# Optimization experiments

Measured on AMD Instinct MI355X. Metric: run time of the kernel, lower is better.

Reference implementation:

```python
import jax, jax.numpy as jnp
from jax import lax
import numpy as np

DEPTH = 10  # matches init depth; n_nodes = 2**DEPTH - 1 = 1023


def setup_inputs() -> dict:
    key = jax.random.key(0)
    k1, k2, k3 = jax.random.split(key, 3)
    B, nIn, nOut = 65536, 1024, 1024
    n_nodes = 2 ** DEPTH - 1
    x = jax.random.normal(k1, (B, nIn), dtype=jnp.float32)
    # hyperspherical-shell init: unit-normalized gaussian rows
    w1s = jax.random.normal(k2, (n_nodes, nIn), dtype=jnp.float32)
    w1s = w1s / jnp.linalg.norm(w1s, axis=-1, keepdims=True)
    w2s = jax.random.normal(k3, (n_nodes, nOut), dtype=jnp.float32)
    w2s = w2s / jnp.linalg.norm(w2s, axis=-1, keepdims=True)
    return {"x": x, "w1s": w1s, "w2s": w2s}


def reference(x, w1s, w2s):
    B = x.shape[0]
    nOut = w2s.shape[1]

    def step(carry, _):
        node, y = carry                      # node: [B] int32, y: [B, nOut]
        lam = jnp.einsum('bi,bi->b', x, w1s[node])      # per-sample dot
        y = y + lam[:, None] * w2s[node]                 # accumulate scaled leaf vec
        node = node * 2 + 1 + (lam > 0).astype(node.dtype)  # descend tree
        return (node, y), None

    init = (jnp.zeros((B,), dtype=jnp.int32), jnp.zeros((B, nOut), dtype=x.dtype))
    (_, y), _ = lax.scan(step, init, None, length=DEPTH)
    return y
```

## Files before the change

kernel.cpp:

```cpp
#include <hip/hip_runtime.h>


#define FFF_DEPTH 10
#define N_IN 1024
#define N_OUT 1024
#define N_LEAF 512
#define LEAF_BASE 511
#define BIN_CAP 512

typedef float f32x4 __attribute__((ext_vector_type(4)));

template<int CTRL, int ROW_MASK>
__device__ __forceinline__ float dpp_add(float v) {
    int sh = __builtin_amdgcn_update_dpp(0, __builtin_bit_cast(int, v),
                                         CTRL, ROW_MASK, 0xf, true);
    return v + __builtin_bit_cast(float, sh);
}

__device__ __forceinline__ float wave_sum(float p) {
    p = dpp_add<0x111, 0xf>(p);
    p = dpp_add<0x112, 0xf>(p);
    p = dpp_add<0x114, 0xf>(p);
    p = dpp_add<0x118, 0xf>(p);
    p = dpp_add<0x142, 0xa>(p);
    p = dpp_add<0x143, 0xc>(p);
    return __builtin_bit_cast(float,
        __builtin_amdgcn_readlane(__builtin_bit_cast(int, p), 63));
}

__device__ __forceinline__ void store_stream(f32x4 v, f32x4* addr) {
    asm volatile("global_store_dwordx4 %0, %1, off sc0 sc1 nt"
                 :: "v"(addr), "v"(v) : "memory");
}

__global__ __launch_bounds__(256, 4) void route_kernel(
    const float* __restrict__ x,
    const float* __restrict__ w1s,
    float* __restrict__ lams16,
    int* __restrict__ bins,
    int* __restrict__ cnt,
    int B)
{
    const int lane = threadIdx.x & 63;
    const int wv = threadIdx.x >> 6;
    const int b0 = (blockIdx.x * 4 + wv) * 2;
    const int b1 = b0 + 1;
    if (b0 >= B) return;

    const f32x4* xa = reinterpret_cast<const f32x4*>(x + (size_t)b0 * N_IN);
    const f32x4* xb = reinterpret_cast<const f32x4*>(x + (size_t)b1 * N_IN);
    f32x4 xv0[4], xv1[4];
    #pragma unroll
    for (int c = 0; c < 4; ++c) {
        xv0[c] = __builtin_nontemporal_load(&xa[c * 64 + lane]);
        xv1[c] = __builtin_nontemporal_load(&xb[c * 64 + lane]);
    }

    float myl = 0.f;
    const int sel = lane & 15;

    int n0 = 0, n1 = 0;
    #pragma unroll
    for (int d = 0; d < FFF_DEPTH; ++d) {
        const f32x4* wa = reinterpret_cast<const f32x4*>(w1s + (size_t)n0 * N_IN);
        const f32x4* wb = reinterpret_cast<const f32x4*>(w1s + (size_t)n1 * N_IN);
        f32x4 w0[4], w1v[4];
        #pragma unroll
        for (int c = 0; c < 4; ++c) { w0[c] = wa[c * 64 + lane]; w1v[c] = wb[c * 64 + lane]; }

        float p0 = 0.f, p1 = 0.f, p2 = 0.f, p3 = 0.f;
        float q0 = 0.f, q1 = 0.f, q2 = 0.f, q3 = 0.f;
        #pragma unroll
        for (int c = 0; c < 4; ++c) {
            p0 += xv0[c][0] * w0[c][0];  q0 += xv1[c][0] * w1v[c][0];
            p1 += xv0[c][1] * w0[c][1];  q1 += xv1[c][1] * w1v[c][1];
            p2 += xv0[c][2] * w0[c][2];  q2 += xv1[c][2] * w1v[c][2];
            p3 += xv0[c][3] * w0[c][3];  q3 += xv1[c][3] * w1v[c][3];
        }
        float lam0 = wave_sum((p0 + p1) + (p2 + p3));
        float lam1 = wave_sum((q0 + q1) + (q2 + q3));

        const float pick = (lane < 16) ? lam0 : lam1;
        myl = (sel == d) ? pick : myl;

        n0 = n0 * 2 + 1 + (lam0 > 0.f ? 1 : 0);
        n1 = n1 * 2 + 1 + (lam1 > 0.f ? 1 : 0);
    }

    if (lane < 32) lams16[(size_t)b0 * 16 + lane] = (sel < FFF_DEPTH) ? myl : 0.f;

    if (lane == 0) {
        int l0 = ((n0 - 1) >> 1) - LEAF_BASE;
        int p = atomicAdd(&cnt[l0], 1);
        if (p < BIN_CAP) bins[l0 * BIN_CAP + p] = b0;
    }
    if (lane == 1) {
        int l1 = ((n1 - 1) >> 1) - LEAF_BASE;
        int p = atomicAdd(&cnt[l1], 1);
        if (p < BIN_CAP) bins[l1 * BIN_CAP + p] = b1;
    }
}

__global__ __launch_bounds__(256, 4) void accum_kernel(
    const float* __restrict__ w2s,
    const float* __restrict__ lams16,
    const int* __restrict__ bins,
    const int* __restrict__ cnt,
    float* __restrict__ y)
{
    __shared__ float lds[FFF_DEPTH * N_OUT];
    const int leaf = blockIdx.x >> 1;
    const int half = blockIdx.x & 1;

    int nodes[FFF_DEPTH];
    int n = LEAF_BASE + leaf;
    #pragma unroll
    for (int d = FFF_DEPTH - 1; d >= 0; --d) { nodes[d] = n; n = (n - 1) >> 1; }

    const int tid = threadIdx.x;
    f32x4* lds4 = reinterpret_cast<f32x4*>(lds);
    #pragma unroll
    for (int d = 0; d < FFF_DEPTH; ++d) {
        const f32x4* src = reinterpret_cast<const f32x4*>(w2s + (size_t)nodes[d] * N_OUT);
        lds4[d * 256 + tid] = src[tid];
    }
    __syncthreads();

    int nsamp = cnt[leaf];
    if (nsamp > BIN_CAP) nsamp = BIN_CAP;
    const int nh = (nsamp + 1) >> 1;
    const int rs = half ? nh : 0;
    const int re = half ? nsamp : nh;

    const int lane = tid & 63, wv = tid >> 6;
    const int* mybin = bins + leaf * BIN_CAP;

    int p = rs + wv;

    for (; p + 4 < re; p += 8) {
        const int b0 = __builtin_amdgcn_readfirstlane(mybin[p]);
        const int b1 = __builtin_amdgcn_readfirstlane(mybin[p + 4]);
        const float lv0 = lams16[(size_t)b0 * 16 + (lane & 15)];
        const float lv1 = lams16[(size_t)b1 * 16 + (lane & 15)];

        f32x4 a0[4], a1[4];
        #pragma unroll
        for (int c = 0; c < 4; ++c) { a0[c] = (f32x4)0.f; a1[c] = (f32x4)0.f; }
        #pragma unroll
        for (int d = 0; d < FFF_DEPTH; ++d) {
            const float s0 = __builtin_bit_cast(float,
                __builtin_amdgcn_readlane(__builtin_bit_cast(int, lv0), d));
            const float s1 = __builtin_bit_cast(float,
                __builtin_amdgcn_readlane(__builtin_bit_cast(int, lv1), d));
            #pragma unroll
            for (int c = 0; c < 4; ++c) {
                const f32x4 w = lds4[d * 256 + c * 64 + lane];
                a0[c] += s0 * w;
                a1[c] += s1 * w;
            }
        }
        f32x4* y0 = reinterpret_cast<f32x4*>(y + (size_t)b0 * N_OUT);
        f32x4* y1 = reinterpret_cast<f32x4*>(y + (size_t)b1 * N_OUT);
        #pragma unroll
        for (int c = 0; c < 4; ++c) {
            store_stream(a0[c], &y0[c * 64 + lane]);
            store_stream(a1[c], &y1[c * 64 + lane]);
        }
    }

    for (; p < re; p += 4) {
        const int b = __builtin_amdgcn_readfirstlane(mybin[p]);
        const float lv = lams16[(size_t)b * 16 + (lane & 15)];
        f32x4 acc[4];
        #pragma unroll
        for (int c = 0; c < 4; ++c) acc[c] = (f32x4)0.f;
        #pragma unroll
        for (int d = 0; d < FFF_DEPTH; ++d) {
            const float s = __builtin_bit_cast(float,
                __builtin_amdgcn_readlane(__builtin_bit_cast(int, lv), d));
            #pragma unroll
            for (int c = 0; c < 4; ++c) acc[c] += s * lds4[d * 256 + c * 64 + lane];
        }
        f32x4* y4 = reinterpret_cast<f32x4*>(y + (size_t)b * N_OUT);
        #pragma unroll
        for (int c = 0; c < 4; ++c) store_stream(acc[c], &y4[c * 64 + lane]);
    }
}

__global__ __launch_bounds__(256, 4) void fff_mono_kernel(
    const float* __restrict__ x, const float* __restrict__ w1s,
    const float* __restrict__ w2s, float* __restrict__ y, int B)
{
    const int lane = threadIdx.x & 63;
    const int b = blockIdx.x * 4 + (threadIdx.x >> 6);
    if (b >= B) return;
    const f32x4* x4 = reinterpret_cast<const f32x4*>(x + (size_t)b * N_IN);
    f32x4 xv[4], acc[4];
    #pragma unroll
    for (int c = 0; c < 4; ++c) { xv[c] = __builtin_nontemporal_load(&x4[c*64+lane]); acc[c] = (f32x4)0.f; }
    int node = 0;
    #pragma unroll
    for (int d = 0; d < FFF_DEPTH; ++d) {
        const f32x4* w1 = reinterpret_cast<const f32x4*>(w1s + (size_t)node * N_IN);
        const f32x4* w2 = reinterpret_cast<const f32x4*>(w2s + (size_t)node * N_OUT);
        f32x4 w[4], v[4];
        #pragma unroll
        for (int c = 0; c < 4; ++c) { w[c] = w1[c*64+lane]; v[c] = w2[c*64+lane]; }
        float p0=0,p1=0,p2=0,p3=0;
        #pragma unroll
        for (int c = 0; c < 4; ++c) {
            p0 += xv[c][0]*w[c][0]; p1 += xv[c][1]*w[c][1];
            p2 += xv[c][2]*w[c][2]; p3 += xv[c][3]*w[c][3];
        }
        float lam = wave_sum((p0+p1)+(p2+p3));
        #pragma unroll
        for (int c = 0; c < 4; ++c) acc[c] += lam * v[c];
        node = node * 2 + 1 + (lam > 0.f ? 1 : 0);
    }
    f32x4* y4 = reinterpret_cast<f32x4*>(y + (size_t)b * N_OUT);
    #pragma unroll
    for (int c = 0; c < 4; ++c) y4[c*64+lane] = acc[c];
}

extern "C" void kernel_launch(void* const* d_in, const int* in_sizes, int n_in,
                              void* d_out, int out_size, void* d_ws, size_t ws_size,
                              hipStream_t stream) {
    const float* x   = (const float*)d_in[0];
    const float* w1s = (const float*)d_in[1];
    const float* w2s = (const float*)d_in[2];
    float* y = (float*)d_out;
    const int B = in_sizes[0] / N_IN;

    float* lams16 = (float*)d_ws;
    int*   bins   = (int*)(lams16 + (size_t)B * 16);
    int*   cnt    = bins + (size_t)N_LEAF * BIN_CAP;
    const size_t need = ((size_t)B * 16 + (size_t)N_LEAF * BIN_CAP + N_LEAF) * 4;

    if (ws_size < need) {
        fff_mono_kernel<<<(B + 3) / 4, 256, 0, stream>>>(x, w1s, w2s, y, B);
        return;
    }

    hipMemsetAsync(cnt, 0, N_LEAF * sizeof(int), stream);
    route_kernel<<<B / 8, 256, 0, stream>>>(x, w1s, lams16, bins, cnt, B);
    accum_kernel<<<2 * N_LEAF, 256, 0, stream>>>(w2s, lams16, bins, cnt, y);
}
```

Before: 205.6 us.

## Stage top tree-level router weights in LDS with persistent route blocks

The routing kernel becomes persistent: 256 blocks of 1024 threads loop over sample pairs, and each block first copies the first 31 w1s rows (tree levels 0-4) into 124 KB of shared memory. The first five levels read those weights from LDS and the last five still read from global memory. The memset is replaced by a tiny zeroing kernel, and the fallback path's y stores become nontemporal streaming stores. The large LDS footprint limits each CU to one route block, and the 1024-thread launch bound may force register spilling.

```diff
diff --git a/kernel.cpp b/kernel.cpp
--- a/kernel.cpp
+++ b/kernel.cpp
@@ -7,6 +7,9 @@
 #define N_LEAF 512
 #define LEAF_BASE 511
 #define BIN_CAP 512
+#define N_STAGE 31
+#define ROUTE_THREADS 1024
+#define ROUTE_BLOCKS 256
 
 typedef float f32x4 __attribute__((ext_vector_type(4)));
 
@@ -33,7 +36,32 @@
                  :: "v"(addr), "v"(v) : "memory");
 }
 
-__global__ __launch_bounds__(256, 4) void route_kernel(
+#define ROUTE_LEVEL_BODY(dd, wa, wb)                                          \
+    {                                                                         \
+        f32x4 w0[4], w1v[4];                                                  \
+        _Pragma("unroll")                                                     \
+        for (int c = 0; c < 4; ++c) {                                         \
+            w0[c] = (wa)[c * 64 + lane];                                      \
+            w1v[c] = (wb)[c * 64 + lane];                                     \
+        }                                                                     \
+        float p0 = 0.f, p1 = 0.f, p2 = 0.f, p3 = 0.f;                         \
+        float q0 = 0.f, q1 = 0.f, q2 = 0.f, q3 = 0.f;                         \
+        _Pragma("unroll")                                                     \
+        for (int c = 0; c < 4; ++c) {                                         \
+            p0 += xv0[c][0] * w0[c][0];  q0 += xv1[c][0] * w1v[c][0];         \
+            p1 += xv0[c][1] * w0[c][1];  q1 += xv1[c][1] * w1v[c][1];         \
+            p2 += xv0[c][2] * w0[c][2];  q2 += xv1[c][2] * w1v[c][2];         \
+            p3 += xv0[c][3] * w0[c][3];  q3 += xv1[c][3] * w1v[c][3];         \
+        }                                                                     \
+        const float lam0 = wave_sum((p0 + p1) + (p2 + p3));                   \
+        const float lam1 = wave_sum((q0 + q1) + (q2 + q3));                   \
+        const float pick = (lane < 16) ? lam0 : lam1;                         \
+        myl = (sel == (dd)) ? pick : myl;                                     \
+        n0 = n0 * 2 + 1 + (lam0 > 0.f ? 1 : 0);                               \
+        n1 = n1 * 2 + 1 + (lam1 > 0.f ? 1 : 0);                               \
+    }
+
+__global__ __launch_bounds__(ROUTE_THREADS, 4) void route_kernel(
     const float* __restrict__ x,
     const float* __restrict__ w1s,
     float* __restrict__ lams16,
@@ -41,64 +69,67 @@
     int* __restrict__ cnt,
     int B)
 {
+    extern __shared__ float w1_lds[];
+
+    {
+        f32x4* dst = reinterpret_cast<f32x4*>(w1_lds);
+        const f32x4* src = reinterpret_cast<const f32x4*>(w1s);
+        for (int i = threadIdx.x; i < N_STAGE * 256; i += ROUTE_THREADS)
+            dst[i] = src[i];
+    }
+    __syncthreads();
+
     const int lane = threadIdx.x & 63;
-    const int wv = threadIdx.x >> 6;
-    const int b0 = (blockIdx.x * 4 + wv) * 2;
-    const int b1 = b0 + 1;
-    if (b0 >= B) return;
-
-    const f32x4* xa = reinterpret_cast<const f32x4*>(x + (size_t)b0 * N_IN);
-    const f32x4* xb = reinterpret_cast<const f32x4*>(x + (size_t)b1 * N_IN);
-    f32x4 xv0[4], xv1[4];
-    #pragma unroll
-    for (int c = 0; c < 4; ++c) {
-        xv0[c] = __builtin_nontemporal_load(&xa[c * 64 + lane]);
-        xv1[c] = __builtin_nontemporal_load(&xb[c * 64 + lane]);
-    }
-
-    float myl = 0.f;
+    const int wslot = blockIdx.x * (ROUTE_THREADS / 64) + (threadIdx.x >> 6);
+    const int wstride = gridDim.x * (ROUTE_THREADS / 64);
+    const int npairs = B >> 1;
     const int sel = lane & 15;
 
-    int n0 = 0, n1 = 0;
-    #pragma unroll
-    for (int d = 0; d < FFF_DEPTH; ++d) {
-        const f32x4* wa = reinterpret_cast<const f32x4*>(w1s + (size_t)n0 * N_IN);
-        const f32x4* wb = reinterpret_cast<const f32x4*>(w1s + (size_t)n1 * N_IN);
-        f32x4 w0[4], w1v[4];
-        #pragma unroll
-        for (int c = 0; c < 4; ++c) { w0[c] = wa[c * 64 + lane]; w1v[c] = wb[c * 64 + lane]; }
-
-        float p0 = 0.f, p1 = 0.f, p2 = 0.f, p3 = 0.f;
-        float q0 = 0.f, q1 = 0.f, q2 = 0.f, q3 = 0.f;
+    for (int pr = wslot; pr < npairs; pr += wstride) {
+        const int b0 = pr * 2, b1 = b0 + 1;
+
+        const f32x4* xa = reinterpret_cast<const f32x4*>(x + (size_t)b0 * N_IN);
+        const f32x4* xb = reinterpret_cast<const f32x4*>(x + (size_t)b1 * N_IN);
+        f32x4 xv0[4], xv1[4];
         #pragma unroll
         for (int c = 0; c < 4; ++c) {
-            p0 += xv0[c][0] * w0[c][0];  q0 += xv1[c][0] * w1v[c][0];
-            p1 += xv0[c][1] * w0[c][1];  q1 += xv1[c][1] * w1v[c][1];
-            p2 += xv0[c][2] * w0[c][2];  q2 += xv1[c][2] * w1v[c][2];
-            p3 += xv0[c][3] * w0[c][3];  q3 += xv1[c][3] * w1v[c][3];
-        }
-        float lam0 = wave_sum((p0 + p1) + (p2 + p3));
-        float lam1 = wave_sum((q0 + q1) + (q2 + q3));
-
-        const float pick = (lane < 16) ? lam0 : lam1;
-        myl = (sel == d) ? pick : myl;
-
-        n0 = n0 * 2 + 1 + (lam0 > 0.f ? 1 : 0);
-        n1 = n1 * 2 + 1 + (lam1 > 0.f ? 1 : 0);
-    }
-
-    if (lane < 32) lams16[(size_t)b0 * 16 + lane] = (sel < FFF_DEPTH) ? myl : 0.f;
-
-    if (lane == 0) {
-        int l0 = ((n0 - 1) >> 1) - LEAF_BASE;
-        int p = atomicAdd(&cnt[l0], 1);
-        if (p < BIN_CAP) bins[l0 * BIN_CAP + p] = b0;
-    }
-    if (lane == 1) {
-        int l1 = ((n1 - 1) >> 1) - LEAF_BASE;
-        int p = atomicAdd(&cnt[l1], 1);
-        if (p < BIN_CAP) bins[l1 * BIN_CAP + p] = b1;
-    }
+            xv0[c] = __builtin_nontemporal_load(&xa[c * 64 + lane]);
+            xv1[c] = __builtin_nontemporal_load(&xb[c * 64 + lane]);
+        }
+
+        float myl = 0.f;
+        int n0 = 0, n1 = 0;
+
+        #pragma unroll
+        for (int d = 0; d < 5; ++d) {
+            const f32x4* wa = reinterpret_cast<const f32x4*>(w1_lds + n0 * N_IN);
+            const f32x4* wb = reinterpret_cast<const f32x4*>(w1_lds + n1 * N_IN);
+            ROUTE_LEVEL_BODY(d, wa, wb)
+        }
+        #pragma unroll
+        for (int d = 5; d < FFF_DEPTH; ++d) {
+            const f32x4* wa = reinterpret_cast<const f32x4*>(w1s + (size_t)n0 * N_IN);
+            const f32x4* wb = reinterpret_cast<const f32x4*>(w1s + (size_t)n1 * N_IN);
+            ROUTE_LEVEL_BODY(d, wa, wb)
+        }
+
+        if (lane < 32) lams16[(size_t)b0 * 16 + lane] = (sel < FFF_DEPTH) ? myl : 0.f;
+
+        if (lane == 0) {
+            int l0 = ((n0 - 1) >> 1) - LEAF_BASE;
+            int p = atomicAdd(&cnt[l0], 1);
+            if (p < BIN_CAP) bins[l0 * BIN_CAP + p] = b0;
+        }
+        if (lane == 1) {
+            int l1 = ((n1 - 1) >> 1) - LEAF_BASE;
+            int p = atomicAdd(&cnt[l1], 1);
+            if (p < BIN_CAP) bins[l1 * BIN_CAP + p] = b1;
+        }
+    }
+}
+
+__global__ void zero_cnt_kernel(int* __restrict__ cnt) {
+    cnt[threadIdx.x] = 0;
 }
 
 __global__ __launch_bounds__(256, 4) void accum_kernel(
@@ -219,7 +250,7 @@
     }
     f32x4* y4 = reinterpret_cast<f32x4*>(y + (size_t)b * N_OUT);
     #pragma unroll
-    for (int c = 0; c < 4; ++c) y4[c*64+lane] = acc[c];
+    for (int c = 0; c < 4; ++c) store_stream(acc[c], &y4[c*64+lane]);
 }
 
 extern "C" void kernel_launch(void* const* d_in, const int* in_sizes, int n_in,
@@ -241,7 +272,8 @@
         return;
     }
 
-    hipMemsetAsync(cnt, 0, N_LEAF * sizeof(int), stream);
-    route_kernel<<<B / 8, 256, 0, stream>>>(x, w1s, lams16, bins, cnt, B);
+    zero_cnt_kernel<<<1, N_LEAF, 0, stream>>>(cnt);
+    route_kernel<<<ROUTE_BLOCKS, ROUTE_THREADS, N_STAGE * N_IN * sizeof(float), stream>>>(
+        x, w1s, lams16, bins, cnt, B);
     accum_kernel<<<2 * N_LEAF, 256, 0, stream>>>(w2s, lams16, bins, cnt, y);
 }
```

Result: faster. 174.0 us (-15.4%).
